# Kernel optimization log

Hardware: AMD Instinct MI355X
Metric: run time of the kernel (lower is better)

## Reference

```python
import jax, jax.numpy as jnp
import numpy as np


def setup_inputs() -> dict:
    key = jax.random.key(0)
    k1, k2 = jax.random.split(key)
    B, N, D = 4, 2048, 1024
    context = jax.random.normal(k1, (B, N, D), dtype=jnp.float32)
    # Dense(embedding_dim*3): kernel [D, 3D], bias [3D] (glorot-ish scale)
    W_qkv = jax.random.normal(k2, (D, 3 * D), dtype=jnp.float32) * (1.0 / np.sqrt(D))
    b_qkv = jnp.zeros((3 * D,), dtype=jnp.float32)
    return {"context": context, "W_qkv": W_qkv, "b_qkv": b_qkv}


def reference(context, W_qkv, b_qkv):
    B, N, D = context.shape
    qkv = context @ W_qkv + b_qkv                       # [B, N, 3D]
    q, k, v = jnp.split(qkv, 3, axis=-1)                # each [B, N, D]
    scores = jnp.einsum("bnd,bmd->bnm", q, k)           # [B, N, N]
    # Faithful quirk: original divides by sqrt(scores.shape[-1]) == sqrt(N)
    scores = scores / jnp.asarray(np.sqrt(N), dtype=scores.dtype)
    causal = jnp.tril(jnp.ones((N, N), dtype=jnp.float32))  # lower-triangular
    scores = jnp.where(causal == 0, -jnp.inf, scores)
    probs = jax.nn.softmax(scores, axis=-1)             # [B, N, N]
    out = jnp.einsum("bnm,bmd->bnd", probs, v)          # [B, N, D]
    return out
```

## Files before the change

### kernel.cpp

```cpp
#include <hip/hip_runtime.h>
#include <cstdint>
#include <cstddef>


typedef __attribute__((ext_vector_type(8))) __bf16 bf16x8;
typedef __attribute__((ext_vector_type(4))) float f32x4;

__device__ inline unsigned short f2bf(float f) {
  unsigned u = __float_as_uint(f);
  u = (u + 0x7FFFu + ((u >> 16) & 1u)) >> 16;
  return (unsigned short)u;
}

__device__ inline void gld16(const void* g, void* l) {
  __builtin_amdgcn_global_load_lds(
      (const __attribute__((address_space(1))) unsigned int*)g,
      (__attribute__((address_space(3))) unsigned int*)l, 16, 0, 0);
}

__device__ inline void compute_tiles(const unsigned short* As, const unsigned short* Bs,
                                     int lane, int ry, int rx, f32x4 acc[4][4]) {
#pragma unroll
  for (int kk = 0; kk < 64; kk += 32) {
    const int cbase = (kk >> 3) + (lane >> 4);
    const int csw = ((cbase ^ (lane & 7)) << 3);
    bf16x8 a[4], b[4];
#pragma unroll
    for (int mi = 0; mi < 4; mi++)
      a[mi] = *(const bf16x8*)&As[(ry + mi * 16 + (lane & 15)) * 64 + csw];
#pragma unroll
    for (int nj = 0; nj < 4; nj++)
      b[nj] = *(const bf16x8*)&Bs[(rx + nj * 16 + (lane & 15)) * 64 + csw];
#pragma unroll
    for (int mi = 0; mi < 4; mi++)
#pragma unroll
      for (int nj = 0; nj < 4; nj++)
        acc[mi][nj] = __builtin_amdgcn_mfma_f32_16x16x32_bf16(b[nj], a[mi], acc[mi][nj], 0, 0, 0);
  }
}

__device__ inline void mma_mainloop(unsigned short* As, unsigned short* Bs,
                                    const unsigned short* Abase, long strideA,
                                    const unsigned short* Bbase, long strideB,
                                    int kIters, f32x4 acc[4][4]) {
  const int lane = threadIdx.x & 63, wave = threadIdx.x >> 6;
  const int ry = (wave >> 1) * 64, rx = (wave & 1) * 64;
  const int lrow = lane >> 3;
  const int lcol = ((lane & 7) ^ lrow) * 8;
#pragma unroll
  for (int mi = 0; mi < 4; mi++)
#pragma unroll
    for (int nj = 0; nj < 4; nj++) acc[mi][nj] = (f32x4)(0.f);
  for (int kt = 0; kt < kIters; kt++) {
    const int k0 = kt * 64;
    __syncthreads();
#pragma unroll
    for (int c = 0; c < 4; c++) {
      const int q = wave * 4 + c;
      const int row = q * 8 + lrow;
      gld16(Abase + (size_t)row * strideA + k0 + lcol, &As[q * 512]);
      gld16(Bbase + (size_t)row * strideB + k0 + lcol, &Bs[q * 512]);
    }
    __syncthreads();
    compute_tiles(As, Bs, lane, ry, rx, acc);
  }
}

__device__ inline void compute_tiles64(const unsigned short* As, const unsigned short* Bs,
                                       int lane, int ry, int rx, f32x4 acc[4][2]) {
#pragma unroll
  for (int kk = 0; kk < 64; kk += 32) {
    const int cbase = (kk >> 3) + (lane >> 4);
    const int csw = ((cbase ^ (lane & 7)) << 3);
    bf16x8 a[4], b[2];
#pragma unroll
    for (int mi = 0; mi < 4; mi++)
      a[mi] = *(const bf16x8*)&As[(ry + mi * 16 + (lane & 15)) * 64 + csw];
#pragma unroll
    for (int nj = 0; nj < 2; nj++)
      b[nj] = *(const bf16x8*)&Bs[(rx + nj * 16 + (lane & 15)) * 64 + csw];
#pragma unroll
    for (int mi = 0; mi < 4; mi++)
#pragma unroll
      for (int nj = 0; nj < 2; nj++)
        acc[mi][nj] = __builtin_amdgcn_mfma_f32_16x16x32_bf16(b[nj], a[mi], acc[mi][nj], 0, 0, 0);
  }
}

__device__ inline void mma_mainloop64(unsigned short* As, unsigned short* Bs,
                                      const unsigned short* Abase, long strideA,
                                      const unsigned short* Bbase, long strideB,
                                      int kIters, f32x4 acc[4][2]) {
  const int lane = threadIdx.x & 63, wave = threadIdx.x >> 6;
  const int ry = (wave >> 1) * 64, rx = (wave & 1) * 32;
  const int lrow = lane >> 3;
  const int lcol = ((lane & 7) ^ lrow) * 8;
#pragma unroll
  for (int mi = 0; mi < 4; mi++)
#pragma unroll
    for (int nj = 0; nj < 2; nj++) acc[mi][nj] = (f32x4)(0.f);
  for (int kt = 0; kt < kIters; kt++) {
    const int k0 = kt * 64;
    __syncthreads();
#pragma unroll
    for (int c = 0; c < 4; c++) {
      const int q = wave * 4 + c;
      const int row = q * 8 + lrow;
      gld16(Abase + (size_t)row * strideA + k0 + lcol, &As[q * 512]);
    }
#pragma unroll
    for (int c = 0; c < 2; c++) {
      const int q = wave * 2 + c;
      const int row = q * 8 + lrow;
      gld16(Bbase + (size_t)row * strideB + k0 + lcol, &Bs[q * 512]);
    }
    __syncthreads();
    compute_tiles64(As, Bs, lane, ry, rx, acc);
  }
}

__global__ void k_prep(const float* __restrict__ x, unsigned short* __restrict__ y,
                       const float* __restrict__ W, unsigned short* __restrict__ Wt,
                       float* __restrict__ lsum) {
  __shared__ unsigned short sm[64 * 65];
  const int bid = blockIdx.x;
  if (bid < 2048) {
#pragma unroll
    for (int k = 0; k < 4; k++) {
      const int i = bid * 1024 + k * 256 + threadIdx.x;
      float4 v = ((const float4*)x)[i];
      ushort4 o;
      o.x = f2bf(v.x); o.y = f2bf(v.y); o.z = f2bf(v.z); o.w = f2bf(v.w);
      ((ushort4*)y)[i] = o;
    }
  } else if (bid < 2816) {
    const int t = bid - 2048;
    const int n0 = (t % 48) * 64;
    const int k0 = (t / 48) * 64;
    for (int i = threadIdx.x; i < 4096; i += 256) {
      int r = i >> 6, c = i & 63;
      sm[c * 65 + r] = f2bf(W[(size_t)(k0 + r) * 3072 + n0 + c]);
    }
    __syncthreads();
    for (int i = threadIdx.x; i < 4096; i += 256) {
      int r = i >> 6, c = i & 63;
      Wt[(size_t)(n0 + r) * 1024 + k0 + c] = sm[r * 65 + c];
    }
  } else {
#pragma unroll
    for (int k = 0; k < 8; k++)
      ((float4*)lsum)[k * 256 + threadIdx.x] = (float4)(0.f);
  }
}

__global__ __launch_bounds__(256) void k_gemm_qk(const unsigned short* __restrict__ A,
                                                 const unsigned short* __restrict__ Wt,
                                                 const float* __restrict__ bias,
                                                 unsigned short* __restrict__ qk) {
  __shared__ unsigned short As[128 * 64];
  __shared__ unsigned short Bs[128 * 64];
  f32x4 acc[4][4];
  const int tN0 = blockIdx.x * 128;
  const int tM0 = blockIdx.y * 128;
  mma_mainloop(As, Bs, A + (size_t)tM0 * 1024, 1024, Wt + (size_t)tN0 * 1024, 1024, 16, acc);
  const int lane = threadIdx.x & 63, wave = threadIdx.x >> 6;
  const int ry = (wave >> 1) * 64, rx = (wave & 1) * 64;
  const int l16 = lane & 15, rq = lane >> 4;
#pragma unroll
  for (int mi = 0; mi < 4; mi++) {
    const int m = tM0 + ry + mi * 16 + l16;
#pragma unroll
    for (int nj = 0; nj < 4; nj++) {
      const int n = tN0 + rx + nj * 16 + rq * 4;
      const float4 bv = *(const float4*)&bias[n];
      ushort4 o;
      o.x = f2bf(acc[mi][nj][0] + bv.x);
      o.y = f2bf(acc[mi][nj][1] + bv.y);
      o.z = f2bf(acc[mi][nj][2] + bv.z);
      o.w = f2bf(acc[mi][nj][3] + bv.w);
      *(ushort4*)&qk[(size_t)m * 2048 + n] = o;
    }
  }
}

__global__ __launch_bounds__(256) void k_vscores(
    const unsigned short* __restrict__ A, const unsigned short* __restrict__ Wt,
    const float* __restrict__ bias, unsigned short* __restrict__ vT,
    const unsigned short* __restrict__ qk, unsigned short* __restrict__ P,
    float* __restrict__ l, float scale) {
  __shared__ unsigned short smem[16384];
  unsigned short* As = smem;
  unsigned short* Bs = smem + 8192;
  const int bid = blockIdx.x;
  const int lane = threadIdx.x & 63, wave = threadIdx.x >> 6;
  if (bid < 512) {
    f32x4 acc[4][4];
    const int tN0 = (bid & 7) * 128;
    const int tM0 = (bid >> 3) * 128;
    mma_mainloop(As, Bs, A + (size_t)tM0 * 1024, 1024,
                 Wt + (size_t)(2048 + tN0) * 1024, 1024, 16, acc);
    int tM0v = tM0;
    asm volatile("" : "+v"(tM0v));
    const int ry = (wave >> 1) * 64, rx = (wave & 1) * 64;
    const int l16 = lane & 15, rq = lane >> 4;
#pragma unroll
    for (int mi = 0; mi < 4; mi++) {
      const int m = tM0v + ry + mi * 16 + l16;
      const int b = m >> 11, ns = m & 2047;
#pragma unroll
      for (int nj = 0; nj < 4; nj++) {
        const int d0 = tN0 + rx + nj * 16 + rq * 4;
        const float4 bv = *(const float4*)&bias[2048 + d0];
#pragma unroll
        for (int r = 0; r < 4; r++)
          vT[((size_t)(b * 1024 + d0 + r)) * 2048 + ns] =
              f2bf(acc[mi][nj][r] + ((const float*)&bv)[r]);
      }
    }
  } else {
    const int idx = bid - 512;
    const int b = idx & 3;
    const int t = idx >> 2;
    int qb = (int)((sqrtf(4.0f * (float)t + 1.0f) - 1.0f) * 0.5f);
    while (qb * (qb + 1) > t) qb--;
    while ((qb + 1) * (qb + 2) <= t) qb++;
    const int kb2 = t - qb * (qb + 1);
    f32x4 acc[4][2];
    const unsigned short* Aq = qk + ((size_t)(b * 2048 + qb * 128)) * 2048;
    const unsigned short* Bk = qk + ((size_t)(b * 2048 + kb2 * 64)) * 2048 + 1024;
    mma_mainloop64(As, Bs, Aq, 2048, Bk, 2048, 16, acc);
    const int ry = (wave >> 1) * 64, rx = (wave & 1) * 32;
    const int l16 = lane & 15, rq = lane >> 4;
    unsigned short* Pb = P + ((size_t)(b * 2048 + qb * 128)) * 2048 + (size_t)kb2 * 64;
    float* lb = l + b * 2048 + qb * 128;
#pragma unroll
    for (int mi = 0; mi < 4; mi++) {
      const int m_local = ry + mi * 16 + l16;
      const int qi = qb * 128 + m_local;
      float rowpart = 0.f;
#pragma unroll
      for (int nj = 0; nj < 2; nj++) {
        const int n_base = rx + nj * 16 + rq * 4;
        ushort4 o;
        float p;
#pragma unroll
        for (int r = 0; r < 4; r++) {
          const int kj = kb2 * 64 + n_base + r;
          p = (kj <= qi) ? __expf(acc[mi][nj][r] * scale) : 0.f;
          rowpart += p;
          ((unsigned short*)&o)[r] = f2bf(p);
        }
        *(ushort4*)&Pb[(size_t)m_local * 2048 + n_base] = o;
      }
      rowpart += __shfl_xor(rowpart, 16, 64);
      rowpart += __shfl_xor(rowpart, 32, 64);
      if (rq == 0) atomicAdd(&lb[m_local], rowpart);
    }
  }
}

__global__ __launch_bounds__(256) void k_pv(const unsigned short* __restrict__ P,
                                            const unsigned short* __restrict__ vT,
                                            const float* __restrict__ l,
                                            float* __restrict__ out) {
  __shared__ unsigned short As[128 * 64];
  __shared__ unsigned short Bs[64 * 64];
  const int t = blockIdx.x;
  const int qb = 15 - (t >> 6);
  const int r = t & 63;
  const int db2 = r >> 2;
  const int b = r & 3;
  f32x4 acc[4][2];
  const unsigned short* Ap = P + ((size_t)(b * 2048 + qb * 128)) * 2048;
  const unsigned short* Bv = vT + ((size_t)(b * 1024 + db2 * 64)) * 2048;
  mma_mainloop64(As, Bs, Ap, 2048, Bv, 2048, (qb + 1) * 2, acc);
  const int lane = threadIdx.x & 63, wave = threadIdx.x >> 6;
  const int ry = (wave >> 1) * 64, rx = (wave & 1) * 32;
  const int l16 = lane & 15, rq = lane >> 4;
  const float* lb = l + b * 2048 + qb * 128;
  float* ob = out + ((size_t)(b * 2048 + qb * 128)) * 1024 + db2 * 64;
#pragma unroll
  for (int mi = 0; mi < 4; mi++) {
    const int m_local = ry + mi * 16 + l16;
    const float inv = 1.0f / lb[m_local];
#pragma unroll
    for (int nj = 0; nj < 2; nj++) {
      const int n_base = rx + nj * 16 + rq * 4;
      float4 o;
      o.x = acc[mi][nj][0] * inv;
      o.y = acc[mi][nj][1] * inv;
      o.z = acc[mi][nj][2] * inv;
      o.w = acc[mi][nj][3] * inv;
      *(float4*)&ob[(size_t)m_local * 1024 + n_base] = o;
    }
  }
}


extern "C" void kernel_launch(void* const* d_in, const int* in_sizes, int n_in,
                              void* d_out, int out_size, void* d_ws, size_t ws_size,
                              hipStream_t stream) {
  const float* ctx  = (const float*)d_in[0];
  const float* W    = (const float*)d_in[1];
  const float* bias = (const float*)d_in[2];
  float* out = (float*)d_out;

  char* ws = (char*)d_ws;
  unsigned short* Actx = (unsigned short*)(ws + 0);
  unsigned short* Wt   = (unsigned short*)(ws + 16777216);
  unsigned short* qk   = (unsigned short*)(ws + 23068672);
  unsigned short* vT   = (unsigned short*)(ws + 56623104);
  unsigned short* P    = (unsigned short*)(ws + 73400320);
  float*          lsum = (float*)(ws + 106954752);

  k_prep<<<2817, 256, 0, stream>>>(ctx, Actx, W, Wt, lsum);
  k_gemm_qk<<<dim3(16, 64), 256, 0, stream>>>(Actx, Wt, bias, qk);
  k_vscores<<<1600, 256, 0, stream>>>(Actx, Wt, bias, vT, qk, P, lsum,
                                      0.022097086912079608f);
  k_pv<<<1024, 256, 0, stream>>>(P, vT, lsum, out);
}
```

Before: 238.7 us.

## Move V projection into the QKV GEMM kernel and split scores into own kernel

The V-projection GEMM blocks move from the scores kernel into the Q/K projection kernel, giving one 1536-block QKV GEMM launch followed by a dedicated causal scores kernel. Previously the V GEMM tiles shared a launch with the scores tiles, which mixes heavy and light blocks. The new split makes each launch uniform and lets the scores kernel use a smaller LDS footprint (64-row B tile), which can raise occupancy. The cost is that V work no longer overlaps with score computation inside one launch.

```diff
diff --git a/kernel.cpp b/kernel.cpp
--- a/kernel.cpp
+++ b/kernel.cpp
@@ -153,50 +153,42 @@
   }
 }
 
-__global__ __launch_bounds__(256) void k_gemm_qk(const unsigned short* __restrict__ A,
-                                                 const unsigned short* __restrict__ Wt,
-                                                 const float* __restrict__ bias,
-                                                 unsigned short* __restrict__ qk) {
+__global__ __launch_bounds__(256) void k_gemm_qkv(
+    const unsigned short* __restrict__ A, const unsigned short* __restrict__ Wt,
+    const float* __restrict__ bias, unsigned short* __restrict__ qk,
+    unsigned short* __restrict__ vT) {
   __shared__ unsigned short As[128 * 64];
   __shared__ unsigned short Bs[128 * 64];
-  f32x4 acc[4][4];
-  const int tN0 = blockIdx.x * 128;
-  const int tM0 = blockIdx.y * 128;
-  mma_mainloop(As, Bs, A + (size_t)tM0 * 1024, 1024, Wt + (size_t)tN0 * 1024, 1024, 16, acc);
-  const int lane = threadIdx.x & 63, wave = threadIdx.x >> 6;
-  const int ry = (wave >> 1) * 64, rx = (wave & 1) * 64;
-  const int l16 = lane & 15, rq = lane >> 4;
-#pragma unroll
-  for (int mi = 0; mi < 4; mi++) {
-    const int m = tM0 + ry + mi * 16 + l16;
-#pragma unroll
-    for (int nj = 0; nj < 4; nj++) {
-      const int n = tN0 + rx + nj * 16 + rq * 4;
-      const float4 bv = *(const float4*)&bias[n];
-      ushort4 o;
-      o.x = f2bf(acc[mi][nj][0] + bv.x);
-      o.y = f2bf(acc[mi][nj][1] + bv.y);
-      o.z = f2bf(acc[mi][nj][2] + bv.z);
-      o.w = f2bf(acc[mi][nj][3] + bv.w);
-      *(ushort4*)&qk[(size_t)m * 2048 + n] = o;
-    }
-  }
-}
-
-__global__ __launch_bounds__(256) void k_vscores(
-    const unsigned short* __restrict__ A, const unsigned short* __restrict__ Wt,
-    const float* __restrict__ bias, unsigned short* __restrict__ vT,
-    const unsigned short* __restrict__ qk, unsigned short* __restrict__ P,
-    float* __restrict__ l, float scale) {
-  __shared__ unsigned short smem[16384];
-  unsigned short* As = smem;
-  unsigned short* Bs = smem + 8192;
   const int bid = blockIdx.x;
   const int lane = threadIdx.x & 63, wave = threadIdx.x >> 6;
-  if (bid < 512) {
+  if (bid < 1024) {
     f32x4 acc[4][4];
-    const int tN0 = (bid & 7) * 128;
-    const int tM0 = (bid >> 3) * 128;
+    const int tN0 = (bid & 15) * 128;
+    const int tM0 = (bid >> 4) * 128;
+    mma_mainloop(As, Bs, A + (size_t)tM0 * 1024, 1024,
+                 Wt + (size_t)tN0 * 1024, 1024, 16, acc);
+    const int ry = (wave >> 1) * 64, rx = (wave & 1) * 64;
+    const int l16 = lane & 15, rq = lane >> 4;
+#pragma unroll
+    for (int mi = 0; mi < 4; mi++) {
+      const int m = tM0 + ry + mi * 16 + l16;
+#pragma unroll
+      for (int nj = 0; nj < 4; nj++) {
+        const int n = tN0 + rx + nj * 16 + rq * 4;
+        const float4 bv = *(const float4*)&bias[n];
+        ushort4 o;
+        o.x = f2bf(acc[mi][nj][0] + bv.x);
+        o.y = f2bf(acc[mi][nj][1] + bv.y);
+        o.z = f2bf(acc[mi][nj][2] + bv.z);
+        o.w = f2bf(acc[mi][nj][3] + bv.w);
+        *(ushort4*)&qk[(size_t)m * 2048 + n] = o;
+      }
+    }
+  } else {
+    f32x4 acc[4][4];
+    const int idx = bid - 1024;
+    const int tN0 = (idx & 7) * 128;
+    const int tM0 = (idx >> 3) * 128;
     mma_mainloop(As, Bs, A + (size_t)tM0 * 1024, 1024,
                  Wt + (size_t)(2048 + tN0) * 1024, 1024, 16, acc);
     int tM0v = tM0;
@@ -217,45 +209,50 @@
               f2bf(acc[mi][nj][r] + ((const float*)&bv)[r]);
       }
     }
-  } else {
-    const int idx = bid - 512;
-    const int b = idx & 3;
-    const int t = idx >> 2;
-    int qb = (int)((sqrtf(4.0f * (float)t + 1.0f) - 1.0f) * 0.5f);
-    while (qb * (qb + 1) > t) qb--;
-    while ((qb + 1) * (qb + 2) <= t) qb++;
-    const int kb2 = t - qb * (qb + 1);
-    f32x4 acc[4][2];
-    const unsigned short* Aq = qk + ((size_t)(b * 2048 + qb * 128)) * 2048;
-    const unsigned short* Bk = qk + ((size_t)(b * 2048 + kb2 * 64)) * 2048 + 1024;
-    mma_mainloop64(As, Bs, Aq, 2048, Bk, 2048, 16, acc);
-    const int ry = (wave >> 1) * 64, rx = (wave & 1) * 32;
-    const int l16 = lane & 15, rq = lane >> 4;
-    unsigned short* Pb = P + ((size_t)(b * 2048 + qb * 128)) * 2048 + (size_t)kb2 * 64;
-    float* lb = l + b * 2048 + qb * 128;
-#pragma unroll
-    for (int mi = 0; mi < 4; mi++) {
-      const int m_local = ry + mi * 16 + l16;
-      const int qi = qb * 128 + m_local;
-      float rowpart = 0.f;
-#pragma unroll
-      for (int nj = 0; nj < 2; nj++) {
-        const int n_base = rx + nj * 16 + rq * 4;
-        ushort4 o;
-        float p;
-#pragma unroll
-        for (int r = 0; r < 4; r++) {
-          const int kj = kb2 * 64 + n_base + r;
-          p = (kj <= qi) ? __expf(acc[mi][nj][r] * scale) : 0.f;
-          rowpart += p;
-          ((unsigned short*)&o)[r] = f2bf(p);
-        }
-        *(ushort4*)&Pb[(size_t)m_local * 2048 + n_base] = o;
+  }
+}
+
+__global__ __launch_bounds__(256) void k_scores(const unsigned short* __restrict__ qk,
+                                                unsigned short* __restrict__ P,
+                                                float* __restrict__ l, float scale) {
+  __shared__ unsigned short As[128 * 64];
+  __shared__ unsigned short Bs[64 * 64];
+  const int t = blockIdx.x, b = blockIdx.z;
+  int qb = (int)((sqrtf(4.0f * (float)t + 1.0f) - 1.0f) * 0.5f);
+  while (qb * (qb + 1) > t) qb--;
+  while ((qb + 1) * (qb + 2) <= t) qb++;
+  const int kb2 = t - qb * (qb + 1);
+  f32x4 acc[4][2];
+  const unsigned short* Aq = qk + ((size_t)(b * 2048 + qb * 128)) * 2048;
+  const unsigned short* Bk = qk + ((size_t)(b * 2048 + kb2 * 64)) * 2048 + 1024;
+  mma_mainloop64(As, Bs, Aq, 2048, Bk, 2048, 16, acc);
+  const int lane = threadIdx.x & 63, wave = threadIdx.x >> 6;
+  const int ry = (wave >> 1) * 64, rx = (wave & 1) * 32;
+  const int l16 = lane & 15, rq = lane >> 4;
+  unsigned short* Pb = P + ((size_t)(b * 2048 + qb * 128)) * 2048 + (size_t)kb2 * 64;
+  float* lb = l + b * 2048 + qb * 128;
+#pragma unroll
+  for (int mi = 0; mi < 4; mi++) {
+    const int m_local = ry + mi * 16 + l16;
+    const int qi = qb * 128 + m_local;
+    float rowpart = 0.f;
+#pragma unroll
+    for (int nj = 0; nj < 2; nj++) {
+      const int n_base = rx + nj * 16 + rq * 4;
+      ushort4 o;
+      float p;
+#pragma unroll
+      for (int r = 0; r < 4; r++) {
+        const int kj = kb2 * 64 + n_base + r;
+        p = (kj <= qi) ? __expf(acc[mi][nj][r] * scale) : 0.f;
+        rowpart += p;
+        ((unsigned short*)&o)[r] = f2bf(p);
       }
-      rowpart += __shfl_xor(rowpart, 16, 64);
-      rowpart += __shfl_xor(rowpart, 32, 64);
-      if (rq == 0) atomicAdd(&lb[m_local], rowpart);
-    }
+      *(ushort4*)&Pb[(size_t)m_local * 2048 + n_base] = o;
+    }
+    rowpart += __shfl_xor(rowpart, 16, 64);
+    rowpart += __shfl_xor(rowpart, 32, 64);
+    if (rq == 0) atomicAdd(&lb[m_local], rowpart);
   }
 }
 
@@ -314,8 +311,7 @@
   float*          lsum = (float*)(ws + 106954752);
 
   k_prep<<<2817, 256, 0, stream>>>(ctx, Actx, W, Wt, lsum);
-  k_gemm_qk<<<dim3(16, 64), 256, 0, stream>>>(Actx, Wt, bias, qk);
-  k_vscores<<<1600, 256, 0, stream>>>(Actx, Wt, bias, vT, qk, P, lsum,
-                                      0.022097086912079608f);
+  k_gemm_qkv<<<1536, 256, 0, stream>>>(Actx, Wt, bias, qk, vT);
+  k_scores<<<dim3(272, 1, 4), 256, 0, stream>>>(qk, P, lsum, 0.022097086912079608f);
   k_pv<<<1024, 256, 0, stream>>>(P, vT, lsum, out);
 }
```

Measured after the change: 238.3 us. Within noise of the previous version (-0.2%).
